# Optimization experiments

Hardware: AMD Instinct MI355X
Metric: run time of the kernel (lower is better)

## Reference

```python
import jax, jax.numpy as jnp
import numpy as np

N, CIN, COUT, H, W = 32, 256, 256, 56, 56

def setup_inputs() -> dict:
    key = jax.random.key(0)
    k1, k2, k3 = jax.random.split(key, 3)
    x = jax.random.normal(k1, (N, CIN, H, W), dtype=jnp.float32)
    weight = jax.random.normal(k2, (COUT, CIN, 3, 3), dtype=jnp.float32) * 0.05
    bias = jax.random.normal(k3, (COUT,), dtype=jnp.float32)
    return {"x": x, "weight": weight, "bias": bias}

def reference(x, weight, bias):
    # 3x3 conv, stride=1, padding=1 (SAME), fused bias + ReLU.
    # Winograd F(2x2,3x3) is mathematically identical to direct conv.
    y = jax.lax.conv_general_dilated(
        x, weight,
        window_strides=(1, 1),
        padding=((1, 1), (1, 1)),
        dimension_numbers=("NCHW", "OIHW", "NCHW"),
    )
    return jax.nn.relu(y + bias[None, :, None, None])
```

## Files before the change

### kernel.cpp

```cpp
#include <hip/hip_runtime.h>


#define GLOBAL_AS __attribute__((address_space(1)))
#define LDS_AS __attribute__((address_space(3)))

typedef __attribute__((ext_vector_type(8))) short short8;
typedef __attribute__((ext_vector_type(4))) float f32x4;
typedef __attribute__((ext_vector_type(4))) unsigned int u32x4;

#define CIN   256
#define HWS   3136
#define PTOT  100352
#define KTOT  2304
#define WROWB 4608
#define ZPOFF 1179648
#define XTOFF 1310720
#define WSNEED (XTOFF + (size_t)PTOT * 512)

__device__ __forceinline__ unsigned short f2bf(float f) {
  unsigned u = __builtin_bit_cast(unsigned, f);
  return (unsigned short)((u + 0x7fffu + ((u >> 16) & 1u)) >> 16);
}

__global__ void wcvt_kernel(const float* __restrict__ w, unsigned char* __restrict__ ws) {
  if (blockIdx.x == 0 && threadIdx.x < 128)
    ((unsigned*)(ws + ZPOFF))[threadIdx.x] = 0u;
  int o = blockIdx.x * 256 + threadIdx.x;
  int co = o / KTOT;
  int rr = o - co * KTOT;
  int tap = rr >> 8;
  int ci = rr & 255;
  ((unsigned short*)ws)[o] = f2bf(w[co * KTOT + ci * 9 + tap]);
}

__global__ __launch_bounds__(256) void xcvt_kernel(const float* __restrict__ x,
                                                   unsigned char* __restrict__ ws) {
  __shared__ float lt[64 * 257];
  const int pg0 = blockIdx.x * 64;
  const int n   = pg0 / HWS;
  const int pi0 = pg0 - n * HWS;
  const int t   = threadIdx.x;
  {
    const int px = t & 63;
    const int cg = t >> 6;
    const float* xb = x + ((size_t)n * 256) * HWS + pi0 + px;
#pragma unroll 8
    for (int i = 0; i < 64; ++i) {
      const int c = i * 4 + cg;
      lt[px * 257 + c] = xb[(size_t)c * HWS];
    }
  }
  __syncthreads();
  {
    const int slot = t & 31;
    const int pxw  = t >> 5;
    unsigned char* xt = ws + XTOFF;
#pragma unroll
    for (int i = 0; i < 8; ++i) {
      const int p = i * 8 + pxw;
      const float* r = &lt[p * 257 + slot * 8];
      u32x4 v;
#pragma unroll
      for (int j = 0; j < 4; ++j)
        v[j] = (unsigned)f2bf(r[2 * j]) | ((unsigned)f2bf(r[2 * j + 1]) << 16);
      *(u32x4*)(xt + (size_t)(pg0 + p) * 512 + slot * 16) = v;
    }
  }
}

__global__ __launch_bounds__(256, 2) void conv_kernel(
    const unsigned char* __restrict__ ws, const float* __restrict__ bias,
    float* __restrict__ out) {
  __shared__ __align__(16) unsigned char smem[65536];

  const unsigned char* wb = ws;
  const unsigned char* xt = ws + XTOFF;
  const unsigned char* zp = ws + ZPOFF;

  const int bid = blockIdx.x;
  const int sw  = (bid & 7) * 196 + (bid >> 3);
  const int co0 = (sw & 1) * 128;
  const int p0  = (sw >> 1) * 128;

  const int t    = threadIdx.x;
  const int lane = t & 63;
  const int wave = t >> 6;
  const int wm   = wave & 1;
  const int wn   = wave >> 1;
  const int rl   = lane & 15;
  const int kq   = lane >> 4;
  const int l7   = lane & 7;
  const int l8   = lane >> 3;

  const unsigned chanoff = (unsigned)((l7 * 16) ^ ((l8 & 7) << 4));

  const unsigned char* aG[4];
  long long bG[4];
  int hB[4], wB[4];
#pragma unroll
  for (int i = 0; i < 4; ++i) {
    const int row = wave * 32 + i * 8 + l8;
    aG[i] = wb + (size_t)(co0 + row) * WROWB + chanoff;
    const int pg = p0 + row;
    const int n  = pg / HWS;
    const int pi = pg - n * HWS;
    hB[i] = pi / 56;
    wB[i] = pi - hB[i] * 56;
    bG[i] = (long long)pg * 512 + (long long)chanoff;
  }

  f32x4 acc[4][4];
  const f32x4 zero4 = {0.f, 0.f, 0.f, 0.f};
#pragma unroll
  for (int mi = 0; mi < 4; ++mi)
#pragma unroll
    for (int ni = 0; ni < 4; ++ni) acc[mi][ni] = zero4;

  auto stage = [&](int s, int buf) {
    const int cq  = s / 9;
    const int tap = s - cq * 9;
    const int kh  = tap / 3;
    const int dh  = kh - 1;
    const int dw  = (tap - kh * 3) - 1;
    const int koffA = tap * 512 + cq * 128;
    unsigned char* lb = smem + buf * 32768;
#pragma unroll
    for (int i = 0; i < 4; ++i) {
      __builtin_amdgcn_global_load_lds(
          (const GLOBAL_AS unsigned int*)(aG[i] + koffA),
          (LDS_AS unsigned int*)(lb + (wave * 4 + i) * 1024), 16, 0, 0);
    }
    const long long doff = (long long)(dh * 56 + dw) * 512 + cq * 128;
#pragma unroll
    for (int i = 0; i < 4; ++i) {
      const int hh = hB[i] + dh;
      const int wwi = wB[i] + dw;
      const bool ok = ((unsigned)hh < 56u) && ((unsigned)wwi < 56u);
      const unsigned char* g = ok ? (xt + bG[i] + doff) : zp;
      __builtin_amdgcn_global_load_lds(
          (const GLOBAL_AS unsigned int*)g,
          (LDS_AS unsigned int*)(lb + 16384 + (wave * 4 + i) * 1024), 16, 0, 0);
    }
  };

  unsigned offA[2], offB[2];
#pragma unroll
  for (int ks = 0; ks < 2; ++ks) {
    const unsigned koff = (unsigned)((kq * 16 + ks * 64) ^ (l7 << 4));
    offA[ks] = (unsigned)((wm * 64 + rl) * 128) + koff;
    offB[ks] = (unsigned)((wn * 64 + rl) * 128) + koff;
  }

  auto compute = [&](int buf) {
    const unsigned char* bA = smem + buf * 32768;
    const unsigned char* bB = bA + 16384;
#pragma unroll
    for (int ks = 0; ks < 2; ++ks) {
      short8 a[4], b[4];
#pragma unroll
      for (int mi = 0; mi < 4; ++mi)
        a[mi] = *(const short8*)(bA + offA[ks] + mi * 2048);
#pragma unroll
      for (int ni = 0; ni < 4; ++ni)
        b[ni] = *(const short8*)(bB + offB[ks] + ni * 2048);
#pragma unroll
      for (int mi = 0; mi < 4; ++mi)
#pragma unroll
        for (int ni = 0; ni < 4; ++ni)
          acc[mi][ni] = __builtin_amdgcn_mfma_f32_16x16x32_bf16(
              a[mi], b[ni], acc[mi][ni], 0, 0, 0);
    }
  };

  stage(0, 0);
  __syncthreads();
  int buf = 0;
  for (int s = 0; s < 36; ++s) {
    if (s < 35) stage(s + 1, buf ^ 1);
    compute(buf);
    __syncthreads();
    buf ^= 1;
  }

#pragma unroll
  for (int mi = 0; mi < 4; ++mi) {
    const int row = co0 + wm * 64 + mi * 16 + kq * 4;
    float br[4];
#pragma unroll
    for (int j = 0; j < 4; ++j) br[j] = bias[row + j];
#pragma unroll
    for (int ni = 0; ni < 4; ++ni) {
      const int pgb = p0 + wn * 64 + ni * 16;
      const int n   = pgb / HWS;
      const int pib = pgb - n * HWS;
#pragma unroll
      for (int j = 0; j < 4; ++j) {
        float v = acc[mi][ni][j] + br[j];
        out[(size_t)(n * 256 + row + j) * HWS + pib + rl] = fmaxf(v, 0.f);
      }
    }
  }
}

__global__ void naive_kernel(const float* __restrict__ x, const float* __restrict__ w,
                             const float* __restrict__ bias, float* __restrict__ out) {
  int idx = blockIdx.x * 256 + threadIdx.x;
  if (idx >= 32 * 256 * HWS) return;
  int n  = idx / (256 * HWS);
  int r  = idx - n * 256 * HWS;
  int co = r / HWS;
  int p  = r - co * HWS;
  int h = p / 56, ww = p - h * 56;
  float s = bias[co];
  const float* xb = x + (size_t)n * 256 * HWS;
  const float* wbp = w + (size_t)co * KTOT;
  for (int ci = 0; ci < 256; ++ci) {
    const float* xc = xb + (size_t)ci * HWS;
    const float* wc = wbp + ci * 9;
    for (int kh = 0; kh < 3; ++kh) {
      int hh = h + kh - 1;
      if ((unsigned)hh >= 56u) continue;
      for (int kw = 0; kw < 3; ++kw) {
        int w2 = ww + kw - 1;
        if ((unsigned)w2 >= 56u) continue;
        s += xc[hh * 56 + w2] * wc[kh * 3 + kw];
      }
    }
  }
  out[idx] = fmaxf(s, 0.f);
}

extern "C" void kernel_launch(void* const* d_in, const int* in_sizes, int n_in,
                              void* d_out, int out_size, void* d_ws, size_t ws_size,
                              hipStream_t stream) {
  const float* x    = (const float*)d_in[0];
  const float* w    = (const float*)d_in[1];
  const float* bias = (const float*)d_in[2];
  float* out        = (float*)d_out;

  if (ws_size < WSNEED) {
    hipLaunchKernelGGL(naive_kernel, dim3((32 * 256 * HWS + 255) / 256), dim3(256),
                       0, stream, x, w, bias, out);
    return;
  }
  unsigned char* ws = (unsigned char*)d_ws;
  hipLaunchKernelGGL(wcvt_kernel, dim3(2304), dim3(256), 0, stream, w, ws);
  hipLaunchKernelGGL(xcvt_kernel, dim3(PTOT / 64), dim3(256), 0, stream, x, ws);
  hipLaunchKernelGGL(conv_kernel, dim3(1568), dim3(256), 0, stream, ws, bias, out);
}
```

Measured before the change: 169.0 us.

## Halve K-step to 32 and LDS footprint to raise conv occupancy to 3 blocks

Each pipeline stage now covers a K slice of 32 bf16 values instead of 64, so the double-buffered LDS tile shrinks from 64KB to 32KB and the launch bound asks for 3 blocks per CU. The staging thread mapping and the LDS XOR swizzle are rebuilt for 64-byte rows, and the main loop becomes 72 stages with unroll disabled. The aim is more resident waves to hide global-load latency. In exchange there are twice as many barriers and half as many MFMAs between syncs, and the tighter register budget may cause spills.

```diff
diff --git a/kernel.cpp b/kernel.cpp
--- a/kernel.cpp
+++ b/kernel.cpp
@@ -68,10 +68,10 @@
   }
 }
 
-__global__ __launch_bounds__(256, 2) void conv_kernel(
+__global__ __launch_bounds__(256, 3) void conv_kernel(
     const unsigned char* __restrict__ ws, const float* __restrict__ bias,
     float* __restrict__ out) {
-  __shared__ __align__(16) unsigned char smem[65536];
+  __shared__ __align__(16) unsigned char smem[32768];
 
   const unsigned char* wb = ws;
   const unsigned char* xt = ws + XTOFF;
@@ -89,24 +89,23 @@
   const int wn   = wave >> 1;
   const int rl   = lane & 15;
   const int kq   = lane >> 4;
-  const int l7   = lane & 7;
-  const int l8   = lane >> 3;
-
-  const unsigned chanoff = (unsigned)((l7 * 16) ^ ((l8 & 7) << 4));
-
-  const unsigned char* aG[4];
-  long long bG[4];
-  int hB[4], wB[4];
-#pragma unroll
-  for (int i = 0; i < 4; ++i) {
-    const int row = wave * 32 + i * 8 + l8;
-    aG[i] = wb + (size_t)(co0 + row) * WROWB + chanoff;
+
+  const int srow = t >> 2;
+  const unsigned swzs = (unsigned)((((t & 3) ^ (srow & 3)) << 4));
+
+  const unsigned char* aG[2];
+  long long bG[2];
+  int hB[2], wBp[2];
+#pragma unroll
+  for (int op = 0; op < 2; ++op) {
+    const int row = op * 64 + srow;
+    aG[op] = wb + (size_t)(co0 + row) * WROWB + swzs;
     const int pg = p0 + row;
     const int n  = pg / HWS;
     const int pi = pg - n * HWS;
-    hB[i] = pi / 56;
-    wB[i] = pi - hB[i] * 56;
-    bG[i] = (long long)pg * 512 + (long long)chanoff;
+    hB[op]  = pi / 56;
+    wBp[op] = pi - hB[op] * 56;
+    bG[op]  = (long long)pg * 512 + (long long)swzs;
   }
 
   f32x4 acc[4][4];
@@ -117,66 +116,65 @@
     for (int ni = 0; ni < 4; ++ni) acc[mi][ni] = zero4;
 
   auto stage = [&](int s, int buf) {
-    const int cq  = s / 9;
-    const int tap = s - cq * 9;
+    const int cq  = s / 18;
+    const int r   = s - cq * 18;
+    const int tap = r >> 1;
+    const int kh2 = r & 1;
     const int kh  = tap / 3;
     const int dh  = kh - 1;
     const int dw  = (tap - kh * 3) - 1;
-    const int koffA = tap * 512 + cq * 128;
-    unsigned char* lb = smem + buf * 32768;
-#pragma unroll
-    for (int i = 0; i < 4; ++i) {
+    const unsigned koffA = (unsigned)(tap * 512 + cq * 128 + kh2 * 64);
+    unsigned char* lb = smem + buf * 16384;
+#pragma unroll
+    for (int op = 0; op < 2; ++op)
       __builtin_amdgcn_global_load_lds(
-          (const GLOBAL_AS unsigned int*)(aG[i] + koffA),
-          (LDS_AS unsigned int*)(lb + (wave * 4 + i) * 1024), 16, 0, 0);
-    }
-    const long long doff = (long long)(dh * 56 + dw) * 512 + cq * 128;
-#pragma unroll
-    for (int i = 0; i < 4; ++i) {
-      const int hh = hB[i] + dh;
-      const int wwi = wB[i] + dw;
+          (const GLOBAL_AS unsigned int*)(aG[op] + koffA),
+          (LDS_AS unsigned int*)(lb + op * 4096 + (t >> 6) * 1024), 16, 0, 0);
+    const long long doff = (long long)(dh * 56 + dw) * 512 + cq * 128 + kh2 * 64;
+#pragma unroll
+    for (int op = 0; op < 2; ++op) {
+      const int hh  = hB[op] + dh;
+      const int wwi = wBp[op] + dw;
       const bool ok = ((unsigned)hh < 56u) && ((unsigned)wwi < 56u);
-      const unsigned char* g = ok ? (xt + bG[i] + doff) : zp;
+      const unsigned char* g = ok ? (xt + bG[op] + doff) : zp;
       __builtin_amdgcn_global_load_lds(
           (const GLOBAL_AS unsigned int*)g,
-          (LDS_AS unsigned int*)(lb + 16384 + (wave * 4 + i) * 1024), 16, 0, 0);
+          (LDS_AS unsigned int*)(lb + 8192 + op * 4096 + (t >> 6) * 1024), 16, 0, 0);
     }
   };
 
-  unsigned offA[2], offB[2];
-#pragma unroll
-  for (int ks = 0; ks < 2; ++ks) {
-    const unsigned koff = (unsigned)((kq * 16 + ks * 64) ^ (l7 << 4));
-    offA[ks] = (unsigned)((wm * 64 + rl) * 128) + koff;
-    offB[ks] = (unsigned)((wn * 64 + rl) * 128) + koff;
+  const unsigned krd = (unsigned)((kq * 16) ^ ((rl & 3) << 4));
+  unsigned offA[4], offB[4];
+#pragma unroll
+  for (int i = 0; i < 4; ++i) {
+    offA[i] = (unsigned)((wm * 64 + i * 16 + rl) * 64) + krd;
+    offB[i] = (unsigned)((wn * 64 + i * 16 + rl) * 64) + krd;
   }
 
   auto compute = [&](int buf) {
-    const unsigned char* bA = smem + buf * 32768;
-    const unsigned char* bB = bA + 16384;
-#pragma unroll
-    for (int ks = 0; ks < 2; ++ks) {
-      short8 a[4], b[4];
-#pragma unroll
-      for (int mi = 0; mi < 4; ++mi)
-        a[mi] = *(const short8*)(bA + offA[ks] + mi * 2048);
+    const unsigned char* bA = smem + buf * 16384;
+    const unsigned char* bB = bA + 8192;
+    short8 av[4], bv[4];
+#pragma unroll
+    for (int mi = 0; mi < 4; ++mi)
+      av[mi] = *(const short8*)(bA + offA[mi]);
+#pragma unroll
+    for (int ni = 0; ni < 4; ++ni)
+      bv[ni] = *(const short8*)(bB + offB[ni]);
+#pragma unroll
+    for (int mi = 0; mi < 4; ++mi)
 #pragma unroll
       for (int ni = 0; ni < 4; ++ni)
-        b[ni] = *(const short8*)(bB + offB[ks] + ni * 2048);
-#pragma unroll
-      for (int mi = 0; mi < 4; ++mi)
-#pragma unroll
-        for (int ni = 0; ni < 4; ++ni)
-          acc[mi][ni] = __builtin_amdgcn_mfma_f32_16x16x32_bf16(
-              a[mi], b[ni], acc[mi][ni], 0, 0, 0);
-    }
+        acc[mi][ni] = __builtin_amdgcn_mfma_f32_16x16x32_bf16(
+            av[mi], bv[ni], acc[mi][ni], 0, 0, 0);
   };
 
   stage(0, 0);
   __syncthreads();
   int buf = 0;
-  for (int s = 0; s < 36; ++s) {
-    if (s < 35) stage(s + 1, buf ^ 1);
+#pragma unroll 1
+  for (int s = 0; s < 72; ++s) {
+    if (s < 71) stage(s + 1, buf ^ 1);
     compute(buf);
     __syncthreads();
     buf ^= 1;
```

After: 183.5 us. 1.09x slower.

## Use 8-wave blocks with triple-buffered LDS pipeline and raised MFMA priority

Applied to the files above, without the earlier changes.

Doubles the conv block to 512 threads (8 waves), each wave now computing a 64x32 sub-tile of the same 128x128 output tile. Replaces the double-buffered loop, which did a full __syncthreads per step, with a three-buffer LDS ring (96KB): loads run two stages ahead, and each step ends with a partial s_waitcnt vmcnt plus s_barrier. MFMA sections are wrapped in s_setprio to favour matrix issue. The aim is to hide global-to-LDS latency better. In exchange, the larger LDS footprint likely allows only one block per CU, and each wave does more LDS reads per MFMA.

```diff
diff --git a/kernel.cpp b/kernel.cpp
--- a/kernel.cpp
+++ b/kernel.cpp
@@ -68,10 +68,10 @@
   }
 }
 
-__global__ __launch_bounds__(256, 2) void conv_kernel(
+__global__ __launch_bounds__(512, 2) void conv_kernel(
     const unsigned char* __restrict__ ws, const float* __restrict__ bias,
     float* __restrict__ out) {
-  __shared__ __align__(16) unsigned char smem[65536];
+  __shared__ __align__(16) unsigned char smem[98304];
 
   const unsigned char* wb = ws;
   const unsigned char* xt = ws + XTOFF;
@@ -94,92 +94,102 @@
 
   const unsigned chanoff = (unsigned)((l7 * 16) ^ ((l8 & 7) << 4));
 
-  const unsigned char* aG[4];
-  long long bG[4];
-  int hB[4], wB[4];
-#pragma unroll
-  for (int i = 0; i < 4; ++i) {
-    const int row = wave * 32 + i * 8 + l8;
+  const unsigned char* aG[2];
+  long long bG[2];
+  int hB[2], wBp[2];
+#pragma unroll
+  for (int i = 0; i < 2; ++i) {
+    const int row = wave * 16 + i * 8 + l8;
     aG[i] = wb + (size_t)(co0 + row) * WROWB + chanoff;
     const int pg = p0 + row;
     const int n  = pg / HWS;
     const int pi = pg - n * HWS;
-    hB[i] = pi / 56;
-    wB[i] = pi - hB[i] * 56;
-    bG[i] = (long long)pg * 512 + (long long)chanoff;
-  }
-
-  f32x4 acc[4][4];
+    hB[i]  = pi / 56;
+    wBp[i] = pi - hB[i] * 56;
+    bG[i]  = (long long)pg * 512 + (long long)chanoff;
+  }
+
+  f32x4 acc[4][2];
   const f32x4 zero4 = {0.f, 0.f, 0.f, 0.f};
 #pragma unroll
   for (int mi = 0; mi < 4; ++mi)
 #pragma unroll
-    for (int ni = 0; ni < 4; ++ni) acc[mi][ni] = zero4;
-
-  auto stage = [&](int s, int buf) {
+    for (int ni = 0; ni < 2; ++ni) acc[mi][ni] = zero4;
+
+  auto stage = [&](int s, unsigned bo) {
     const int cq  = s / 9;
     const int tap = s - cq * 9;
     const int kh  = tap / 3;
     const int dh  = kh - 1;
     const int dw  = (tap - kh * 3) - 1;
-    const int koffA = tap * 512 + cq * 128;
-    unsigned char* lb = smem + buf * 32768;
-#pragma unroll
-    for (int i = 0; i < 4; ++i) {
+    const unsigned koffA = (unsigned)(tap * 512 + cq * 128);
+    unsigned char* lb = smem + bo;
+#pragma unroll
+    for (int i = 0; i < 2; ++i)
       __builtin_amdgcn_global_load_lds(
           (const GLOBAL_AS unsigned int*)(aG[i] + koffA),
-          (LDS_AS unsigned int*)(lb + (wave * 4 + i) * 1024), 16, 0, 0);
-    }
+          (LDS_AS unsigned int*)(lb + (wave * 2 + i) * 1024), 16, 0, 0);
     const long long doff = (long long)(dh * 56 + dw) * 512 + cq * 128;
 #pragma unroll
-    for (int i = 0; i < 4; ++i) {
-      const int hh = hB[i] + dh;
-      const int wwi = wB[i] + dw;
+    for (int i = 0; i < 2; ++i) {
+      const int hh  = hB[i] + dh;
+      const int wwi = wBp[i] + dw;
       const bool ok = ((unsigned)hh < 56u) && ((unsigned)wwi < 56u);
-      const unsigned char* g = ok ? (xt + bG[i] + doff) : zp;
+      const unsigned char* g = ok ? (xt + bG[i] + doff) : (zp + chanoff);
       __builtin_amdgcn_global_load_lds(
           (const GLOBAL_AS unsigned int*)g,
-          (LDS_AS unsigned int*)(lb + 16384 + (wave * 4 + i) * 1024), 16, 0, 0);
+          (LDS_AS unsigned int*)(lb + 16384 + (wave * 2 + i) * 1024), 16, 0, 0);
     }
   };
 
-  unsigned offA[2], offB[2];
-#pragma unroll
-  for (int ks = 0; ks < 2; ++ks) {
-    const unsigned koff = (unsigned)((kq * 16 + ks * 64) ^ (l7 << 4));
-    offA[ks] = (unsigned)((wm * 64 + rl) * 128) + koff;
-    offB[ks] = (unsigned)((wn * 64 + rl) * 128) + koff;
-  }
-
-  auto compute = [&](int buf) {
-    const unsigned char* bA = smem + buf * 32768;
+  unsigned krd[2];
+  krd[0] = (unsigned)((kq * 16) ^ (l7 << 4));
+  krd[1] = (unsigned)((kq * 16 + 64) ^ (l7 << 4));
+  unsigned offA[4], offB[2];
+#pragma unroll
+  for (int i = 0; i < 4; ++i)
+    offA[i] = (unsigned)((wm * 64 + i * 16 + rl) * 128);
+#pragma unroll
+  for (int i = 0; i < 2; ++i)
+    offB[i] = (unsigned)((wn * 32 + i * 16 + rl) * 128);
+
+  auto compute = [&](unsigned bo) {
+    const unsigned char* bA = smem + bo;
     const unsigned char* bB = bA + 16384;
 #pragma unroll
     for (int ks = 0; ks < 2; ++ks) {
-      short8 a[4], b[4];
+      short8 av[4], bv[2];
 #pragma unroll
       for (int mi = 0; mi < 4; ++mi)
-        a[mi] = *(const short8*)(bA + offA[ks] + mi * 2048);
-#pragma unroll
-      for (int ni = 0; ni < 4; ++ni)
-        b[ni] = *(const short8*)(bB + offB[ks] + ni * 2048);
+        av[mi] = *(const short8*)(bA + offA[mi] + krd[ks]);
+#pragma unroll
+      for (int ni = 0; ni < 2; ++ni)
+        bv[ni] = *(const short8*)(bB + offB[ni] + krd[ks]);
+      __builtin_amdgcn_s_setprio(1);
 #pragma unroll
       for (int mi = 0; mi < 4; ++mi)
 #pragma unroll
-        for (int ni = 0; ni < 4; ++ni)
+        for (int ni = 0; ni < 2; ++ni)
           acc[mi][ni] = __builtin_amdgcn_mfma_f32_16x16x32_bf16(
-              a[mi], b[ni], acc[mi][ni], 0, 0, 0);
+              av[mi], bv[ni], acc[mi][ni], 0, 0, 0);
+      __builtin_amdgcn_s_setprio(0);
     }
   };
 
-  stage(0, 0);
-  __syncthreads();
-  int buf = 0;
+  stage(0, 0u);
+  stage(1, 32768u);
+
+  unsigned b0 = 0u, b1 = 32768u, b2 = 65536u;
+#pragma unroll 1
   for (int s = 0; s < 36; ++s) {
-    if (s < 35) stage(s + 1, buf ^ 1);
-    compute(buf);
-    __syncthreads();
-    buf ^= 1;
+    if (s < 35) {
+      asm volatile("s_waitcnt vmcnt(4)\n\ts_barrier" ::: "memory");
+    } else {
+      asm volatile("s_waitcnt vmcnt(0)\n\ts_barrier" ::: "memory");
+    }
+    if (s + 2 < 36) stage(s + 2, b2);
+    compute(b0);
+    const unsigned tmp = b0; b0 = b1; b1 = b2; b2 = tmp;
   }
 
 #pragma unroll
@@ -189,8 +199,8 @@
 #pragma unroll
     for (int j = 0; j < 4; ++j) br[j] = bias[row + j];
 #pragma unroll
-    for (int ni = 0; ni < 4; ++ni) {
-      const int pgb = p0 + wn * 64 + ni * 16;
+    for (int ni = 0; ni < 2; ++ni) {
+      const int pgb = p0 + wn * 32 + ni * 16;
       const int n   = pgb / HWS;
       const int pib = pgb - n * HWS;
 #pragma unroll
@@ -246,5 +256,5 @@
   unsigned char* ws = (unsigned char*)d_ws;
   hipLaunchKernelGGL(wcvt_kernel, dim3(2304), dim3(256), 0, stream, w, ws);
   hipLaunchKernelGGL(xcvt_kernel, dim3(PTOT / 64), dim3(256), 0, stream, x, ws);
-  hipLaunchKernelGGL(conv_kernel, dim3(1568), dim3(256), 0, stream, ws, bias, out);
-}
+  hipLaunchKernelGGL(conv_kernel, dim3(1568), dim3(512), 0, stream, ws, bias, out);
+}
```

New measurement: 187.9 us. +11.2%, slower.

## Use zero-padded input layout and fully unrolled K loop with constant offsets

Applied to the files above, without the earlier changes.

The bf16 input is now written into a zero-padded 58x58 NHWC buffer, so the conv main loop drops its per-tap boundary checks and zero-page select. The weights are reordered to match the new K order (channel quarter outer, then tap), and the 36-step K loop is unrolled into two groups of 18 with compile-time LDS and global offsets. This removes index arithmetic and branches from the hot loop. In exchange it adds a memset of the whole padded buffer on every call and makes the code larger.

```diff
diff --git a/kernel.cpp b/kernel.cpp
--- a/kernel.cpp
+++ b/kernel.cpp
@@ -12,10 +12,10 @@
 #define HWS   3136
 #define PTOT  100352
 #define KTOT  2304
-#define WROWB 4608
-#define ZPOFF 1179648
+#define IMGP  3364
 #define XTOFF 1310720
-#define WSNEED (XTOFF + (size_t)PTOT * 512)
+#define XTBYTES ((size_t)32 * IMGP * 512)
+#define WSNEED (XTOFF + XTBYTES)
 
 __device__ __forceinline__ unsigned short f2bf(float f) {
   unsigned u = __builtin_bit_cast(unsigned, f);
@@ -23,14 +23,14 @@
 }
 
 __global__ void wcvt_kernel(const float* __restrict__ w, unsigned char* __restrict__ ws) {
-  if (blockIdx.x == 0 && threadIdx.x < 128)
-    ((unsigned*)(ws + ZPOFF))[threadIdx.x] = 0u;
   int o = blockIdx.x * 256 + threadIdx.x;
   int co = o / KTOT;
-  int rr = o - co * KTOT;
-  int tap = rr >> 8;
-  int ci = rr & 255;
-  ((unsigned short*)ws)[o] = f2bf(w[co * KTOT + ci * 9 + tap]);
+  int r  = o - co * KTOT;
+  int s  = r >> 6;
+  int c  = r & 63;
+  int cq = s / 9;
+  int tap = s - cq * 9;
+  ((unsigned short*)ws)[o] = f2bf(w[co * KTOT + (cq * 64 + c) * 9 + tap]);
 }
 
 __global__ __launch_bounds__(256) void xcvt_kernel(const float* __restrict__ x,
@@ -57,25 +57,30 @@
     unsigned char* xt = ws + XTOFF;
 #pragma unroll
     for (int i = 0; i < 8; ++i) {
-      const int p = i * 8 + pxw;
+      const int p  = i * 8 + pxw;
+      const int pi = pi0 + p;
+      const int h  = pi / 56;
+      const int wcol = pi - h * 56;
+      const size_t gran = (size_t)n * IMGP + (h + 1) * 58 + (wcol + 1);
       const float* r = &lt[p * 257 + slot * 8];
       u32x4 v;
 #pragma unroll
       for (int j = 0; j < 4; ++j)
         v[j] = (unsigned)f2bf(r[2 * j]) | ((unsigned)f2bf(r[2 * j + 1]) << 16);
-      *(u32x4*)(xt + (size_t)(pg0 + p) * 512 + slot * 16) = v;
-    }
-  }
-}
+      *(u32x4*)(xt + gran * 512 + slot * 16) = v;
+    }
+  }
+}
+
+#define DTAP(tp) (((((tp) / 3) - 1) * 58 + ((tp) % 3) - 1) * 512)
 
 __global__ __launch_bounds__(256, 2) void conv_kernel(
     const unsigned char* __restrict__ ws, const float* __restrict__ bias,
     float* __restrict__ out) {
   __shared__ __align__(16) unsigned char smem[65536];
 
-  const unsigned char* wb = ws;
+  const unsigned char* wf = ws;
   const unsigned char* xt = ws + XTOFF;
-  const unsigned char* zp = ws + ZPOFF;
 
   const int bid = blockIdx.x;
   const int sw  = (bid & 7) * 196 + (bid >> 3);
@@ -94,20 +99,27 @@
 
   const unsigned chanoff = (unsigned)((l7 * 16) ^ ((l8 & 7) << 4));
 
-  const unsigned char* aG[4];
-  long long bG[4];
-  int hB[4], wB[4];
+  const unsigned char* aP[4];
+  const unsigned char* bP[4];
 #pragma unroll
   for (int i = 0; i < 4; ++i) {
     const int row = wave * 32 + i * 8 + l8;
-    aG[i] = wb + (size_t)(co0 + row) * WROWB + chanoff;
+    aP[i] = wf + (size_t)(co0 + row) * 4608 + chanoff;
     const int pg = p0 + row;
     const int n  = pg / HWS;
     const int pi = pg - n * HWS;
-    hB[i] = pi / 56;
-    wB[i] = pi - hB[i] * 56;
-    bG[i] = (long long)pg * 512 + (long long)chanoff;
-  }
+    const int h  = pi / 56;
+    const int wc = pi - h * 56;
+    bP[i] = xt + ((size_t)n * IMGP + (h + 1) * 58 + (wc + 1)) * 512 + chanoff;
+  }
+  const unsigned ldsA = (unsigned)(wave * 4096);
+
+  const unsigned krd0 = (unsigned)((kq * 16) ^ (l7 << 4));
+  const unsigned krd1 = (unsigned)((kq * 16 + 64) ^ (l7 << 4));
+  const unsigned char* pA0 = smem + (wm * 64 + rl) * 128 + krd0;
+  const unsigned char* pA1 = smem + (wm * 64 + rl) * 128 + krd1;
+  const unsigned char* pB0 = smem + 16384 + (wn * 64 + rl) * 128 + krd0;
+  const unsigned char* pB1 = smem + 16384 + (wn * 64 + rl) * 128 + krd1;
 
   f32x4 acc[4][4];
   const f32x4 zero4 = {0.f, 0.f, 0.f, 0.f};
@@ -116,71 +128,70 @@
 #pragma unroll
     for (int ni = 0; ni < 4; ++ni) acc[mi][ni] = zero4;
 
-  auto stage = [&](int s, int buf) {
-    const int cq  = s / 9;
-    const int tap = s - cq * 9;
-    const int kh  = tap / 3;
-    const int dh  = kh - 1;
-    const int dw  = (tap - kh * 3) - 1;
-    const int koffA = tap * 512 + cq * 128;
-    unsigned char* lb = smem + buf * 32768;
-#pragma unroll
-    for (int i = 0; i < 4; ++i) {
-      __builtin_amdgcn_global_load_lds(
-          (const GLOBAL_AS unsigned int*)(aG[i] + koffA),
-          (LDS_AS unsigned int*)(lb + (wave * 4 + i) * 1024), 16, 0, 0);
-    }
-    const long long doff = (long long)(dh * 56 + dw) * 512 + cq * 128;
-#pragma unroll
-    for (int i = 0; i < 4; ++i) {
-      const int hh = hB[i] + dh;
-      const int wwi = wB[i] + dw;
-      const bool ok = ((unsigned)hh < 56u) && ((unsigned)wwi < 56u);
-      const unsigned char* g = ok ? (xt + bG[i] + doff) : zp;
-      __builtin_amdgcn_global_load_lds(
-          (const GLOBAL_AS unsigned int*)g,
-          (LDS_AS unsigned int*)(lb + 16384 + (wave * 4 + i) * 1024), 16, 0, 0);
-    }
-  };
-
-  unsigned offA[2], offB[2];
-#pragma unroll
-  for (int ks = 0; ks < 2; ++ks) {
-    const unsigned koff = (unsigned)((kq * 16 + ks * 64) ^ (l7 << 4));
-    offA[ks] = (unsigned)((wm * 64 + rl) * 128) + koff;
-    offB[ks] = (unsigned)((wn * 64 + rl) * 128) + koff;
-  }
-
-  auto compute = [&](int buf) {
-    const unsigned char* bA = smem + buf * 32768;
-    const unsigned char* bB = bA + 16384;
-#pragma unroll
-    for (int ks = 0; ks < 2; ++ks) {
-      short8 a[4], b[4];
-#pragma unroll
-      for (int mi = 0; mi < 4; ++mi)
-        a[mi] = *(const short8*)(bA + offA[ks] + mi * 2048);
-#pragma unroll
-      for (int ni = 0; ni < 4; ++ni)
-        b[ni] = *(const short8*)(bB + offB[ks] + ni * 2048);
-#pragma unroll
-      for (int mi = 0; mi < 4; ++mi)
-#pragma unroll
-        for (int ni = 0; ni < 4; ++ni)
-          acc[mi][ni] = __builtin_amdgcn_mfma_f32_16x16x32_bf16(
-              a[mi], b[ni], acc[mi][ni], 0, 0, 0);
-    }
-  };
-
-  stage(0, 0);
+#define STAGE(DB, AOFF, BD)                                                   \
+  {                                                                           \
+    _Pragma("unroll") for (int i_ = 0; i_ < 4; ++i_)                          \
+        __builtin_amdgcn_global_load_lds(                                     \
+            (const GLOBAL_AS unsigned int*)(aP[i_] + (AOFF)),                 \
+            (LDS_AS unsigned int*)(smem + (DB)*32768 + ldsA + i_ * 1024),     \
+            16, 0, 0);                                                        \
+    _Pragma("unroll") for (int i_ = 0; i_ < 4; ++i_)                          \
+        __builtin_amdgcn_global_load_lds(                                     \
+            (const GLOBAL_AS unsigned int*)(bP[i_] + (BD)),                   \
+            (LDS_AS unsigned int*)(smem + (DB)*32768 + 16384 + ldsA +         \
+                                   i_ * 1024),                                \
+            16, 0, 0);                                                        \
+  }
+
+#define COMP(BUF)                                                             \
+  {                                                                           \
+    short8 av[4], bv[4];                                                      \
+    _Pragma("unroll") for (int mi = 0; mi < 4; ++mi)                          \
+        av[mi] = *(const short8*)(pA0 + (BUF)*32768 + mi * 2048);             \
+    _Pragma("unroll") for (int ni = 0; ni < 4; ++ni)                          \
+        bv[ni] = *(const short8*)(pB0 + (BUF)*32768 + ni * 2048);             \
+    _Pragma("unroll") for (int mi = 0; mi < 4; ++mi)                          \
+      _Pragma("unroll") for (int ni = 0; ni < 4; ++ni)                        \
+          acc[mi][ni] = __builtin_amdgcn_mfma_f32_16x16x32_bf16(              \
+              av[mi], bv[ni], acc[mi][ni], 0, 0, 0);                          \
+    _Pragma("unroll") for (int mi = 0; mi < 4; ++mi)                          \
+        av[mi] = *(const short8*)(pA1 + (BUF)*32768 + mi * 2048);             \
+    _Pragma("unroll") for (int ni = 0; ni < 4; ++ni)                          \
+        bv[ni] = *(const short8*)(pB1 + (BUF)*32768 + ni * 2048);             \
+    _Pragma("unroll") for (int mi = 0; mi < 4; ++mi)                          \
+      _Pragma("unroll") for (int ni = 0; ni < 4; ++ni)                        \
+          acc[mi][ni] = __builtin_amdgcn_mfma_f32_16x16x32_bf16(              \
+              av[mi], bv[ni], acc[mi][ni], 0, 0, 0);                          \
+  }
+
+#define STEPJ(J)                                                              \
+  STAGE(((J) + 1) & 1, ((J) + 1) * 128,                                       \
+        DTAP((((J) + 1) % 9)) + (((J) + 1) / 9) * 128);                       \
+  COMP((J)&1);                                                                \
   __syncthreads();
-  int buf = 0;
-  for (int s = 0; s < 36; ++s) {
-    if (s < 35) stage(s + 1, buf ^ 1);
-    compute(buf);
+
+  STAGE(0, 0, DTAP(0))
+  __syncthreads();
+
+#pragma unroll 1
+  for (int gg = 0; gg < 2; ++gg) {
+    STEPJ(0) STEPJ(1) STEPJ(2) STEPJ(3) STEPJ(4) STEPJ(5) STEPJ(6) STEPJ(7)
+    STEPJ(8) STEPJ(9) STEPJ(10) STEPJ(11) STEPJ(12) STEPJ(13) STEPJ(14)
+    STEPJ(15) STEPJ(16)
+    if (gg == 0) {
+#pragma unroll
+      for (int i = 0; i < 4; ++i) {
+        aP[i] += 2304;
+        bP[i] += 256;
+      }
+      STAGE(0, 0, DTAP(0))
+    }
+    COMP(1)
     __syncthreads();
-    buf ^= 1;
-  }
+  }
+#undef STEPJ
+#undef COMP
+#undef STAGE
 
 #pragma unroll
   for (int mi = 0; mi < 4; ++mi) {
@@ -244,6 +255,7 @@
     return;
   }
   unsigned char* ws = (unsigned char*)d_ws;
+  hipMemsetAsync(ws + XTOFF, 0, XTBYTES, stream);
   hipLaunchKernelGGL(wcvt_kernel, dim3(2304), dim3(256), 0, stream, w, ws);
   hipLaunchKernelGGL(xcvt_kernel, dim3(PTOT / 64), dim3(256), 0, stream, x, ws);
   hipLaunchKernelGGL(conv_kernel, dim3(1568), dim3(256), 0, stream, ws, bias, out);
```

Result: no change. 170.8 us (+1.0%).
